# Kernel optimization log

Measured on AMD Instinct MI355X. Metric: run time of the kernel, lower is better.

The kernel has to match this reference:

```python
import jax, jax.numpy as jnp
import numpy as np

D, NH, DH, NL, NP, NLAYERS, DFF = 256, 8, 32, 3, 4, 6, 1024
SHAPES = ((64, 64), (32, 32), (16, 16))  # (H, W) per level, strides 8/16/32 of a 512px image


def layer_norm(x, g, b):
    m = jnp.mean(x, -1, keepdims=True)
    v = jnp.mean((x - m) ** 2, -1, keepdims=True)
    return (x - m) * jax.lax.rsqrt(v + 1e-5) * g + b


def _ref_points():
    pts = []
    for (h, w) in SHAPES:
        ry = (jnp.arange(h, dtype=jnp.float32) + 0.5) / h
        rx = (jnp.arange(w, dtype=jnp.float32) + 0.5) / w
        yy, xx = jnp.meshgrid(ry, rx, indexing='ij')
        pts.append(jnp.stack([xx.reshape(-1), yy.reshape(-1)], -1))
    return jnp.concatenate(pts, 0)  # [Q, 2] (x, y) normalized; valid_ratios == 1


def _sample_level(value_l, loc, h, w):
    # value_l: [B, NH, h*w, DH]; loc: [B, Q, NH, NP, 2] normalized in [0,1]
    # grid_sample(align_corners=False, padding zeros): pixel = loc*size - 0.5
    B, Q = loc.shape[0], loc.shape[1]
    x = loc[..., 0] * w - 0.5
    y = loc[..., 1] * h - 0.5
    x0f = jnp.floor(x); y0f = jnp.floor(y)
    lx = x - x0f; ly = y - y0f
    x0 = x0f.astype(jnp.int32); y0 = y0f.astype(jnp.int32)
    out = jnp.zeros((B, NH, Q, NP, DH), value_l.dtype)
    corners = ((0, 0, (1 - lx) * (1 - ly)), (1, 0, lx * (1 - ly)),
               (0, 1, (1 - lx) * ly), (1, 1, lx * ly))
    for dx, dy, wgt in corners:
        xi = x0 + dx; yi = y0 + dy
        valid = ((xi >= 0) & (xi < w) & (yi >= 0) & (yi < h)).astype(value_l.dtype)
        idx = jnp.clip(yi, 0, h - 1) * w + jnp.clip(xi, 0, w - 1)        # [B,Q,NH,NP]
        idx_f = jnp.transpose(idx, (0, 2, 1, 3)).reshape(B, NH, Q * NP)
        v = jnp.take_along_axis(value_l, idx_f[..., None], axis=2)       # [B,NH,Q*NP,DH]
        v = v.reshape(B, NH, Q, NP, DH)
        w_f = jnp.transpose(wgt * valid, (0, 2, 1, 3))                   # [B,NH,Q,NP]
        out = out + v * w_f[..., None]
    return out


def setup_inputs():
    key = jax.random.key(0)
    ks = iter(jax.random.split(key, 64))
    d = {}
    B = 4
    for i, (h, w) in enumerate(SHAPES):
        d[f'src{i}'] = jax.random.normal(next(ks), (B, D, h, w), jnp.float32)
        d[f'pos{i}'] = jax.random.normal(next(ks), (B, D, h, w), jnp.float32) * 0.1
    s = 0.02
    p = lambda shape: jax.random.normal(next(ks), shape, jnp.float32) * s
    d['level_embed'] = p((NL, D))
    d['W_off'] = p((NLAYERS, D, NH * NL * NP * 2)); d['b_off'] = p((NLAYERS, NH * NL * NP * 2))
    d['W_attn'] = p((NLAYERS, D, NH * NL * NP));   d['b_attn'] = p((NLAYERS, NH * NL * NP))
    d['W_val'] = p((NLAYERS, D, D)); d['b_val'] = p((NLAYERS, D))
    d['W_out'] = p((NLAYERS, D, D)); d['b_out'] = p((NLAYERS, D))
    d['ln1_g'] = jnp.ones((NLAYERS, D)); d['ln1_b'] = jnp.zeros((NLAYERS, D))
    d['W_ff1'] = p((NLAYERS, D, DFF)); d['b_ff1'] = p((NLAYERS, DFF))
    d['W_ff2'] = p((NLAYERS, DFF, D)); d['b_ff2'] = p((NLAYERS, D))
    d['ln2_g'] = jnp.ones((NLAYERS, D)); d['ln2_b'] = jnp.zeros((NLAYERS, D))
    return d


def reference(src0, src1, src2, pos0, pos1, pos2, level_embed,
              W_off, b_off, W_attn, b_attn, W_val, b_val, W_out, b_out,
              ln1_g, ln1_b, W_ff1, b_ff1, W_ff2, b_ff2, ln2_g, ln2_b):
    srcs = (src0, src1, src2)
    poss = (pos0, pos1, pos2)
    B = src0.shape[0]
    # flatten levels: [B, C, H, W] -> [B, H*W, C]; add per-level embedding to pos
    src = jnp.concatenate([s.reshape(B, D, -1).transpose(0, 2, 1) for s in srcs], 1)
    pos = jnp.concatenate([poss[l].reshape(B, D, -1).transpose(0, 2, 1) + level_embed[l]
                           for l in range(NL)], 1)
    Q = src.shape[1]
    ref = _ref_points()  # [Q, 2]
    x = src
    for i in range(NLAYERS):
        q = x + pos
        off = (q @ W_off[i] + b_off[i]).reshape(B, Q, NH, NL, NP, 2)
        aw = jax.nn.softmax((q @ W_attn[i] + b_attn[i]).reshape(B, Q, NH, NL * NP), -1)
        aw = aw.reshape(B, Q, NH, NL, NP)
        val = (x @ W_val[i] + b_val[i]).reshape(B, Q, NH, DH)
        attn_out = jnp.zeros((B, Q, NH, DH), x.dtype)
        start = 0
        for l, (h, w) in enumerate(SHAPES):
            hw = h * w
            v_l = jnp.transpose(val[:, start:start + hw], (0, 2, 1, 3))  # [B,NH,hw,DH]
            wh = jnp.array([w, h], jnp.float32)
            loc = ref[None, :, None, None, :] + off[:, :, :, l] / wh     # [B,Q,NH,NP,2]
            smp = _sample_level(v_l, loc, h, w)                          # [B,NH,Q,NP,DH]
            attn_out = attn_out + jnp.einsum('bhqpd,bqhp->bqhd', smp, aw[:, :, :, l])
            start += hw
        attn_out = attn_out.reshape(B, Q, D) @ W_out[i] + b_out[i]
        x = layer_norm(x + attn_out, ln1_g[i], ln1_b[i])
        ff = jax.nn.relu(x @ W_ff1[i] + b_ff1[i]) @ W_ff2[i] + b_ff2[i]
        x = layer_norm(x + ff, ln2_g[i], ln2_b[i])
    return x  # memory: [B, Q, D]
```

## Files before the change

kernel.cpp:

```cpp
#include <hip/hip_runtime.h>


#define DMODEL 256
#define NLAYERS 6
#define BATCH 4
#define QTOT 5376
#define MROWS (BATCH * QTOT)

typedef __bf16 bf16x8 __attribute__((ext_vector_type(8)));
typedef __bf16 bf16x4 __attribute__((ext_vector_type(4)));
typedef float floatx4 __attribute__((ext_vector_type(4)));

__global__ __launch_bounds__(256) void flatten_kernel(
    const float* __restrict__ s0, const float* __restrict__ p0,
    const float* __restrict__ s1, const float* __restrict__ p1,
    const float* __restrict__ s2, const float* __restrict__ p2,
    const float* __restrict__ lvl, float* __restrict__ x,
    float* __restrict__ pos, __bf16* __restrict__ xb,
    __bf16* __restrict__ qb) {
  __shared__ float ls[32][33];
  __shared__ float lp[32][33];
  int b = blockIdx.y;
  int tile = blockIdx.x;
  const float* sp; const float* pp; int l, hw, tp, td, qbase;
  if (tile < 1024)      { l = 0; hw = 4096; int t = tile;        td = t & 7; tp = t >> 3; qbase = 0; sp = s0; pp = p0; }
  else if (tile < 1280) { l = 1; hw = 1024; int t = tile - 1024; td = t & 7; tp = t >> 3; qbase = 4096; sp = s1; pp = p1; }
  else                  { l = 2; hw = 256;  int t = tile - 1280; td = t & 7; tp = t >> 3; qbase = 5120; sp = s2; pp = p2; }
  int tx = threadIdx.x & 31, ty = threadIdx.x >> 5;
  int d0 = td * 32, pbase = tp * 32;
#pragma unroll
  for (int r = 0; r < 4; ++r) {
    int dl = r * 8 + ty;
    size_t gi = ((size_t)(b * DMODEL + d0 + dl)) * hw + pbase + tx;
    ls[dl][tx] = sp[gi];
    lp[dl][tx] = pp[gi];
  }
  __syncthreads();
  int d = d0 + tx;
  float lv = lvl[l * DMODEL + d];
#pragma unroll
  for (int r = 0; r < 4; ++r) {
    int pl = r * 8 + ty;
    size_t bq = (size_t)b * QTOT + qbase + pbase + pl;
    float xv = ls[tx][pl];
    float pv = lp[tx][pl] + lv;
    x[bq * DMODEL + d] = xv;
    xb[bq * DMODEL + d] = (__bf16)xv;
    pos[bq * DMODEL + d] = pv;
    qb[bq * DMODEL + d] = (__bf16)(xv + pv);
  }
}

__global__ __launch_bounds__(256) void pack_wt_kernel(
    const float* __restrict__ W, __bf16* __restrict__ Wt, int K, int N) {
  int l = blockIdx.y;
  int idx = blockIdx.x * 256 + threadIdx.x;
  int n = idx / K, k = idx - n * K;
  Wt[(size_t)l * N * K + idx] = (__bf16)W[(size_t)l * K * N + (size_t)k * N + n];
}

__global__ __launch_bounds__(256) void pack_qv_kernel(
    const float* __restrict__ Woff, const float* __restrict__ Wattn,
    const float* __restrict__ Wval,
    const float* __restrict__ boff, const float* __restrict__ battn,
    const float* __restrict__ bval,
    __bf16* __restrict__ Wt, float* __restrict__ bc) {
  int l = blockIdx.y;
  int n = blockIdx.x;
  int k = threadIdx.x;
  float v = 0.f;
  if (n < 192)      v = Woff[((size_t)l * 256 + k) * 192 + n];
  else if (n < 288) v = Wattn[((size_t)l * 256 + k) * 96 + (n - 192)];
  else if (n >= 384) v = Wval[((size_t)l * 256 + k) * 256 + (n - 384)];
  Wt[((size_t)l * 640 + n) * 256 + k] = (__bf16)v;
  if (k == 0) {
    float b = 0.f;
    if (n < 192)      b = boff[l * 192 + n];
    else if (n < 288) b = battn[l * 96 + (n - 192)];
    else if (n >= 384) b = bval[l * 256 + (n - 384)];
    bc[l * 640 + n] = b;
  }
}

#define GEMM_CORE(A_, B_, K_)                                                  \
  for (int k0 = 0; k0 < (K_); k0 += 32) {                                      \
    __syncthreads();                                                           \
    _Pragma("unroll")                                                          \
    for (int cc = 0; cc < 2; ++cc) {                                           \
      int c = wid * 2 + cc;                                                    \
      __builtin_amdgcn_global_load_lds(                                        \
          (__attribute__((address_space(1))) void*)((A_) + (size_t)c * 16 * (K_) + k0), \
          (__attribute__((address_space(3))) void*)(As + c * 512), 16, 0, 0);  \
      __builtin_amdgcn_global_load_lds(                                        \
          (__attribute__((address_space(1))) void*)((B_) + (size_t)c * 16 * (K_) + k0), \
          (__attribute__((address_space(3))) void*)(Bs + c * 512), 16, 0, 0);  \
    }                                                                          \
    __syncthreads();                                                           \
    bf16x8 af[4], bfr[4];                                                      \
    _Pragma("unroll")                                                          \
    for (int i = 0; i < 4; ++i)                                                \
      af[i] = *(const bf16x8*)&As[(wr * 64 + i * 16 + (lane & 15)) * 32 + (lane >> 4) * 8]; \
    _Pragma("unroll")                                                          \
    for (int j = 0; j < 4; ++j)                                                \
      bfr[j] = *(const bf16x8*)&Bs[(wc * 64 + j * 16 + (lane & 15)) * 32 + (lane >> 4) * 8]; \
    _Pragma("unroll")                                                          \
    for (int i = 0; i < 4; ++i)                                                \
      _Pragma("unroll")                                                        \
      for (int j = 0; j < 4; ++j)                                              \
        acc[i][j] = __builtin_amdgcn_mfma_f32_16x16x32_bf16(af[i], bfr[j], acc[i][j], 0, 0, 0); \
  }

template<int RELU, int BF16OUT>
__global__ __launch_bounds__(256) void gemm_bf16_kernel(
    const __bf16* __restrict__ A, const __bf16* __restrict__ Wt,
    const float* __restrict__ bias, float* __restrict__ C,
    __bf16* __restrict__ Cb, int N, int K) {
  __shared__ __bf16 As[128 * 32];
  __shared__ __bf16 Bs[128 * 32];
  int t = threadIdx.x;
  int lane = t & 63, wid = t >> 6;
  int wr = wid >> 1, wc = wid & 1;
  int row0 = blockIdx.y * 128;
  int n0 = blockIdx.x * 128;
  floatx4 acc[4][4] = {};
  int srow = lane >> 2;
  int skoff = (lane & 3) * 8;
  const __bf16* Abase = A + (size_t)(row0 + srow) * K + skoff;
  const __bf16* Bbase = Wt + (size_t)(n0 + srow) * K + skoff;
  GEMM_CORE(Abase, Bbase, K)
  int orow = row0 + wr * 64 + (lane >> 4) * 4;
  int ocol = n0 + wc * 64 + (lane & 15);
#pragma unroll
  for (int i = 0; i < 4; ++i)
#pragma unroll
    for (int j = 0; j < 4; ++j) {
      int col = ocol + j * 16;
      float bv = bias[col];
#pragma unroll
      for (int r = 0; r < 4; ++r) {
        int row = orow + i * 16 + r;
        float v = acc[i][j][r] + bv;
        if (RELU) v = fmaxf(v, 0.f);
        if (BF16OUT) Cb[(size_t)row * N + col] = (__bf16)v;
        else         C[(size_t)row * N + col] = v;
      }
    }
}

__global__ __launch_bounds__(256) void gemm_qv_kernel(
    const __bf16* __restrict__ qb, const __bf16* __restrict__ xb,
    const __bf16* __restrict__ Wt, const float* __restrict__ bias,
    float* __restrict__ qproj, __bf16* __restrict__ valb) {
  __shared__ __bf16 As[128 * 32];
  __shared__ __bf16 Bs[128 * 32];
  int t = threadIdx.x;
  int lane = t & 63, wid = t >> 6;
  int wr = wid >> 1, wc = wid & 1;
  int bn = blockIdx.x;
  int row0 = blockIdx.y * 128;
  int n0 = bn * 128;
  const __bf16* A = (bn < 3) ? qb : xb;
  floatx4 acc[4][4] = {};
  int srow = lane >> 2;
  int skoff = (lane & 3) * 8;
  const __bf16* Abase = A + (size_t)(row0 + srow) * 256 + skoff;
  const __bf16* Bbase = Wt + (size_t)(n0 + srow) * 256 + skoff;
  GEMM_CORE(Abase, Bbase, 256)
  int orow = row0 + wr * 64 + (lane >> 4) * 4;
  int ocol = wc * 64 + (lane & 15);
#pragma unroll
  for (int i = 0; i < 4; ++i)
#pragma unroll
    for (int j = 0; j < 4; ++j) {
      int col = ocol + j * 16;
      float bv = bias[n0 + col];
#pragma unroll
      for (int r = 0; r < 4; ++r) {
        int row = orow + i * 16 + r;
        float v = acc[i][j][r] + bv;
        if (bn < 3) qproj[(size_t)row * 384 + n0 + col] = v;
        else        valb[(size_t)row * 256 + (n0 - 384) + col] = (__bf16)v;
      }
    }
}

__global__ __launch_bounds__(256) void deform_kernel(
    const __bf16* __restrict__ val, const float* __restrict__ qproj,
    __bf16* __restrict__ out) {
  int bq = blockIdx.x * 8 + (threadIdx.x >> 5);
  int b = bq / QTOT, q = bq % QTOT;
  int tq = threadIdx.x & 31;
  int hid = tq >> 2, dq = (tq & 3) * 8;

  int p, wsrc;
  if (q < 4096)      { p = q;        wsrc = 64; }
  else if (q < 5120) { p = q - 4096; wsrc = 32; }
  else               { p = q - 5120; wsrc = 16; }
  float inv = 1.0f / (float)wsrc;
  float refx = ((float)(p % wsrc) + 0.5f) * inv;
  float refy = ((float)(p / wsrc) + 0.5f) * inv;

  const float* base = qproj + (size_t)bq * 384;
  float aw[12], ob[24];
  *(float4*)&aw[0] = *(const float4*)(base + 192 + hid * 12);
  *(float4*)&aw[4] = *(const float4*)(base + 192 + hid * 12 + 4);
  *(float4*)&aw[8] = *(const float4*)(base + 192 + hid * 12 + 8);
#pragma unroll
  for (int i = 0; i < 6; ++i)
    *(float4*)&ob[i * 4] = *(const float4*)(base + hid * 24 + i * 4);

  float mx = -1e30f;
#pragma unroll
  for (int k = 0; k < 12; ++k) mx = fmaxf(mx, aw[k]);
  float s = 0.f;
#pragma unroll
  for (int k = 0; k < 12; ++k) { aw[k] = __expf(aw[k] - mx); s += aw[k]; }
  float invs = 1.0f / s;
#pragma unroll
  for (int k = 0; k < 12; ++k) aw[k] *= invs;

  const __bf16* vb = val + ((size_t)b * QTOT) * DMODEL + hid * 32 + dq;

  const int starts[3] = {0, 4096, 5120};
  const int wls[3] = {64, 32, 16};
  float acc[8] = {};
#pragma unroll
  for (int l = 0; l < 3; ++l) {
    int wl = wls[l], start = starts[l];
    float fwl = (float)wl;
#pragma unroll
    for (int pp = 0; pp < 4; ++pp) {
      float wcomb = aw[l * 4 + pp];
      float fx = refx * fwl + ob[(l * 4 + pp) * 2 + 0] - 0.5f;
      float fy = refy * fwl + ob[(l * 4 + pp) * 2 + 1] - 0.5f;
      float x0f = floorf(fx), y0f = floorf(fy);
      float lx = fx - x0f, ly = fy - y0f;
      int x0 = (int)x0f, y0 = (int)y0f;
#pragma unroll
      for (int c = 0; c < 4; ++c) {
        int dx = c & 1, dy = c >> 1;
        int xi = x0 + dx, yi = y0 + dy;
        if (xi >= 0 && xi < wl && yi >= 0 && yi < wl) {
          float wgt = (dx ? lx : 1.f - lx) * (dy ? ly : 1.f - ly) * wcomb;
          bf16x8 v = *(const bf16x8*)(vb + (size_t)(start + yi * wl + xi) * DMODEL);
#pragma unroll
          for (int e = 0; e < 8; ++e)
            acc[e] = fmaf(wgt, (float)v[e], acc[e]);
        }
      }
    }
  }
  bf16x8 o;
#pragma unroll
  for (int e = 0; e < 8; ++e) o[e] = (__bf16)acc[e];
  *(bf16x8*)(out + (size_t)bq * DMODEL + hid * 32 + dq) = o;
}

__global__ __launch_bounds__(256) void add_ln_kernel(
    const float* __restrict__ x, const float* __restrict__ res,
    const float* __restrict__ g, const float* __restrict__ bta,
    float* __restrict__ xout, __bf16* __restrict__ xb,
    const float* __restrict__ pos, __bf16* __restrict__ qb) {
  int row = blockIdx.x * 4 + (threadIdx.x >> 6);
  int lane = threadIdx.x & 63;
  float4 xv = ((const float4*)(x + (size_t)row * DMODEL))[lane];
  float4 rv = ((const float4*)(res + (size_t)row * DMODEL))[lane];
  xv.x += rv.x; xv.y += rv.y; xv.z += rv.z; xv.w += rv.w;
  float s = xv.x + xv.y + xv.z + xv.w;
  float sq = xv.x * xv.x + xv.y * xv.y + xv.z * xv.z + xv.w * xv.w;
#pragma unroll
  for (int o = 32; o >= 1; o >>= 1) {
    s += __shfl_xor(s, o);
    sq += __shfl_xor(sq, o);
  }
  float mean = s * (1.f / 256.f);
  float var = sq * (1.f / 256.f) - mean * mean;
  float rstd = rsqrtf(var + 1e-5f);
  int c = lane * 4;
  float4 gv = *(const float4*)(g + c);
  float4 bv = *(const float4*)(bta + c);
  float4 o4;
  o4.x = (xv.x - mean) * rstd * gv.x + bv.x;
  o4.y = (xv.y - mean) * rstd * gv.y + bv.y;
  o4.z = (xv.z - mean) * rstd * gv.z + bv.z;
  o4.w = (xv.w - mean) * rstd * gv.w + bv.w;
  ((float4*)(xout + (size_t)row * DMODEL))[lane] = o4;
  bf16x4 ob;
  ob[0] = (__bf16)o4.x; ob[1] = (__bf16)o4.y;
  ob[2] = (__bf16)o4.z; ob[3] = (__bf16)o4.w;
  *(bf16x4*)&xb[(size_t)row * DMODEL + c] = ob;
  if (pos) {
    float4 pv = ((const float4*)(pos + (size_t)row * DMODEL))[lane];
    bf16x4 qv;
    qv[0] = (__bf16)(o4.x + pv.x); qv[1] = (__bf16)(o4.y + pv.y);
    qv[2] = (__bf16)(o4.z + pv.z); qv[3] = (__bf16)(o4.w + pv.w);
    *(bf16x4*)&qb[(size_t)row * DMODEL + c] = qv;
  }
}

extern "C" void kernel_launch(void* const* d_in, const int* in_sizes, int n_in,
                              void* d_out, int out_size, void* d_ws, size_t ws_size,
                              hipStream_t stream) {
  const float* src0 = (const float*)d_in[0];
  const float* pos0 = (const float*)d_in[1];
  const float* src1 = (const float*)d_in[2];
  const float* pos1 = (const float*)d_in[3];
  const float* src2 = (const float*)d_in[4];
  const float* pos2 = (const float*)d_in[5];
  const float* lvl  = (const float*)d_in[6];
  const float* W_off  = (const float*)d_in[7];
  const float* b_off  = (const float*)d_in[8];
  const float* W_attn = (const float*)d_in[9];
  const float* b_attn = (const float*)d_in[10];
  const float* W_val  = (const float*)d_in[11];
  const float* b_val  = (const float*)d_in[12];
  const float* W_out  = (const float*)d_in[13];
  const float* b_out  = (const float*)d_in[14];
  const float* ln1g = (const float*)d_in[15];
  const float* ln1b = (const float*)d_in[16];
  const float* W_ff1 = (const float*)d_in[17];
  const float* b_ff1 = (const float*)d_in[18];
  const float* W_ff2 = (const float*)d_in[19];
  const float* b_ff2 = (const float*)d_in[20];
  const float* ln2g = (const float*)d_in[21];
  const float* ln2b = (const float*)d_in[22];

  const size_t M = (size_t)MROWS;
  char* w = (char*)d_ws;
  float*  x     = (float*)w;                 w += M * 256 * 4;
  float*  pos   = (float*)w;                 w += M * 256 * 4;
  __bf16* xb    = (__bf16*)w;                w += M * 256 * 2;
  __bf16* qb    = (__bf16*)w;                w += M * 256 * 2;
  float*  qproj = (float*)w;                 w += M * 384 * 4;
  __bf16* valb  = (__bf16*)w;                w += M * 256 * 2;
  __bf16* ffh   = (__bf16*)w;                w += M * 1024 * 2;
  __bf16* wqv_t = (__bf16*)w;                w += (size_t)NLAYERS * 640 * 256 * 2;
  __bf16* wout_t= (__bf16*)w;                w += (size_t)NLAYERS * 256 * 256 * 2;
  __bf16* wff1_t= (__bf16*)w;                w += (size_t)NLAYERS * 1024 * 256 * 2;
  __bf16* wff2_t= (__bf16*)w;                w += (size_t)NLAYERS * 256 * 1024 * 2;
  float*  bqv   = (float*)w;                 w += (size_t)NLAYERS * 640 * 4;
  __bf16* attn_bf = qb;
  float*  proj  = (float*)ffh;
  float*  ffres = qproj;

  pack_qv_kernel<<<dim3(640, NLAYERS), 256, 0, stream>>>(
      W_off, W_attn, W_val, b_off, b_attn, b_val, wqv_t, bqv);
  pack_wt_kernel<<<dim3(256, NLAYERS), 256, 0, stream>>>(W_out, wout_t, 256, 256);
  pack_wt_kernel<<<dim3(1024, NLAYERS), 256, 0, stream>>>(W_ff1, wff1_t, 256, 1024);
  pack_wt_kernel<<<dim3(1024, NLAYERS), 256, 0, stream>>>(W_ff2, wff2_t, 1024, 256);

  flatten_kernel<<<dim3(1344, BATCH), 256, 0, stream>>>(
      src0, pos0, src1, pos1, src2, pos2, lvl, x, pos, xb, qb);

  const int MT = MROWS / 128;
  for (int i = 0; i < NLAYERS; ++i) {
    gemm_qv_kernel<<<dim3(5, MT), 256, 0, stream>>>(
        qb, xb, wqv_t + (size_t)i * 640 * 256, bqv + i * 640, qproj, valb);
    deform_kernel<<<MROWS / 8, 256, 0, stream>>>(valb, qproj, attn_bf);
    gemm_bf16_kernel<0, 0><<<dim3(2, MT), 256, 0, stream>>>(
        attn_bf, wout_t + (size_t)i * 256 * 256, b_out + i * 256, proj, nullptr, 256, 256);
    add_ln_kernel<<<MROWS / 4, 256, 0, stream>>>(
        x, proj, ln1g + i * 256, ln1b + i * 256, x, xb, nullptr, nullptr);
    gemm_bf16_kernel<1, 1><<<dim3(8, MT), 256, 0, stream>>>(
        xb, wff1_t + (size_t)i * 1024 * 256, b_ff1 + i * 1024, nullptr, ffh, 1024, 256);
    gemm_bf16_kernel<0, 0><<<dim3(2, MT), 256, 0, stream>>>(
        ffh, wff2_t + (size_t)i * 256 * 1024, b_ff2 + i * 256, ffres, nullptr, 256, 1024);
    float* xdst = (i == NLAYERS - 1) ? (float*)d_out : x;
    add_ln_kernel<<<MROWS / 4, 256, 0, stream>>>(
        x, ffres, ln2g + i * 256, ln2b + i * 256, xdst, xb, pos, qb);
  }
}
```

Before: 1.017 ms.

## Tile weight transposes, branchless deform sampling, bf16 GEMM outputs for residual

Replaces the strided per-element weight pack kernels with 32x32 shared-memory tiled transposes and a separate bias pack. Rewrites the deformable sampling inner loop to clamp indices and zero out-of-range weights, issuing four unconditional loads per point instead of branching per corner. Switches the out-projection and FF2 GEMMs to write bf16, and the add+layernorm kernel to read a bf16 residual, halving that traffic. This costs some residual precision.

```diff
diff --git a/kernel.cpp b/kernel.cpp
--- a/kernel.cpp
+++ b/kernel.cpp
@@ -10,6 +10,11 @@
 typedef __bf16 bf16x8 __attribute__((ext_vector_type(8)));
 typedef __bf16 bf16x4 __attribute__((ext_vector_type(4)));
 typedef float floatx4 __attribute__((ext_vector_type(4)));
+
+#define GLOAD(gp, lp)                                                          \
+  __builtin_amdgcn_global_load_lds(                                            \
+      (__attribute__((address_space(1))) void*)(gp),                           \
+      (__attribute__((address_space(3))) void*)(lp), 16, 0, 0)
 
 __global__ __launch_bounds__(256) void flatten_kernel(
     const float* __restrict__ s0, const float* __restrict__ p0,
@@ -51,35 +56,54 @@
   }
 }
 
-__global__ __launch_bounds__(256) void pack_wt_kernel(
+__global__ __launch_bounds__(256) void pack_t_kernel(
     const float* __restrict__ W, __bf16* __restrict__ Wt, int K, int N) {
-  int l = blockIdx.y;
-  int idx = blockIdx.x * 256 + threadIdx.x;
-  int n = idx / K, k = idx - n * K;
-  Wt[(size_t)l * N * K + idx] = (__bf16)W[(size_t)l * K * N + (size_t)k * N + n];
-}
-
-__global__ __launch_bounds__(256) void pack_qv_kernel(
+  __shared__ float ls[32][33];
+  int l = blockIdx.z;
+  int n0 = blockIdx.x * 32, k0 = blockIdx.y * 32;
+  int tx = threadIdx.x & 31, ty = threadIdx.x >> 5;
+  const float* src = W + (size_t)l * K * N;
+#pragma unroll
+  for (int r = 0; r < 4; ++r)
+    ls[ty + r * 8][tx] = src[(size_t)(k0 + ty + r * 8) * N + n0 + tx];
+  __syncthreads();
+  __bf16* dst = Wt + (size_t)l * N * K;
+#pragma unroll
+  for (int r = 0; r < 4; ++r)
+    dst[(size_t)(n0 + ty + r * 8) * K + k0 + tx] = (__bf16)ls[tx][ty + r * 8];
+}
+
+__global__ __launch_bounds__(256) void pack_qv_t_kernel(
     const float* __restrict__ Woff, const float* __restrict__ Wattn,
-    const float* __restrict__ Wval,
+    const float* __restrict__ Wval, __bf16* __restrict__ Wt) {
+  __shared__ float ls[32][33];
+  int l = blockIdx.z;
+  int tc = blockIdx.x, k0 = blockIdx.y * 32;
+  int tx = threadIdx.x & 31, ty = threadIdx.x >> 5;
+  const float* src; int n0, sn;
+  if (tc < 6)       { src = Woff  + (size_t)l * 256 * 192; n0 = tc * 32;        sn = 192; }
+  else if (tc < 9)  { src = Wattn + (size_t)l * 256 * 96;  n0 = (tc - 6) * 32;  sn = 96;  }
+  else if (tc < 12) { src = nullptr; n0 = 0; sn = 0; }
+  else              { src = Wval  + (size_t)l * 256 * 256; n0 = (tc - 12) * 32; sn = 256; }
+#pragma unroll
+  for (int r = 0; r < 4; ++r)
+    ls[ty + r * 8][tx] = src ? src[(size_t)(k0 + ty + r * 8) * sn + n0 + tx] : 0.f;
+  __syncthreads();
+  __bf16* dst = Wt + (size_t)l * 640 * 256 + (size_t)tc * 32 * 256;
+#pragma unroll
+  for (int r = 0; r < 4; ++r)
+    dst[(size_t)(ty + r * 8) * 256 + k0 + tx] = (__bf16)ls[tx][ty + r * 8];
+}
+
+__global__ __launch_bounds__(640) void pack_bias_kernel(
     const float* __restrict__ boff, const float* __restrict__ battn,
-    const float* __restrict__ bval,
-    __bf16* __restrict__ Wt, float* __restrict__ bc) {
-  int l = blockIdx.y;
-  int n = blockIdx.x;
-  int k = threadIdx.x;
-  float v = 0.f;
-  if (n < 192)      v = Woff[((size_t)l * 256 + k) * 192 + n];
-  else if (n < 288) v = Wattn[((size_t)l * 256 + k) * 96 + (n - 192)];
-  else if (n >= 384) v = Wval[((size_t)l * 256 + k) * 256 + (n - 384)];
-  Wt[((size_t)l * 640 + n) * 256 + k] = (__bf16)v;
-  if (k == 0) {
-    float b = 0.f;
-    if (n < 192)      b = boff[l * 192 + n];
-    else if (n < 288) b = battn[l * 96 + (n - 192)];
-    else if (n >= 384) b = bval[l * 256 + (n - 384)];
-    bc[l * 640 + n] = b;
-  }
+    const float* __restrict__ bval, float* __restrict__ bc) {
+  int l = blockIdx.x, n = threadIdx.x;
+  float b = 0.f;
+  if (n < 192)       b = boff[l * 192 + n];
+  else if (n < 288)  b = battn[l * 96 + (n - 192)];
+  else if (n >= 384) b = bval[l * 256 + (n - 384)];
+  bc[l * 640 + n] = b;
 }
 
 #define GEMM_CORE(A_, B_, K_)                                                  \
@@ -88,12 +112,8 @@
     _Pragma("unroll")                                                          \
     for (int cc = 0; cc < 2; ++cc) {                                           \
       int c = wid * 2 + cc;                                                    \
-      __builtin_amdgcn_global_load_lds(                                        \
-          (__attribute__((address_space(1))) void*)((A_) + (size_t)c * 16 * (K_) + k0), \
-          (__attribute__((address_space(3))) void*)(As + c * 512), 16, 0, 0);  \
-      __builtin_amdgcn_global_load_lds(                                        \
-          (__attribute__((address_space(1))) void*)((B_) + (size_t)c * 16 * (K_) + k0), \
-          (__attribute__((address_space(3))) void*)(Bs + c * 512), 16, 0, 0);  \
+      GLOAD((A_) + (size_t)c * 16 * (K_) + k0, As + c * 512);                  \
+      GLOAD((B_) + (size_t)c * 16 * (K_) + k0, Bs + c * 512);                  \
     }                                                                          \
     __syncthreads();                                                           \
     bf16x8 af[4], bfr[4];                                                      \
@@ -226,27 +246,38 @@
   float acc[8] = {};
 #pragma unroll
   for (int l = 0; l < 3; ++l) {
-    int wl = wls[l], start = starts[l];
+    int wl = wls[l];
     float fwl = (float)wl;
+    const __bf16* vlb = vb + (size_t)starts[l] * DMODEL;
 #pragma unroll
     for (int pp = 0; pp < 4; ++pp) {
-      float wcomb = aw[l * 4 + pp];
+      float awp = aw[l * 4 + pp];
       float fx = refx * fwl + ob[(l * 4 + pp) * 2 + 0] - 0.5f;
       float fy = refy * fwl + ob[(l * 4 + pp) * 2 + 1] - 0.5f;
       float x0f = floorf(fx), y0f = floorf(fy);
       float lx = fx - x0f, ly = fy - y0f;
       int x0 = (int)x0f, y0 = (int)y0f;
-#pragma unroll
-      for (int c = 0; c < 4; ++c) {
-        int dx = c & 1, dy = c >> 1;
-        int xi = x0 + dx, yi = y0 + dy;
-        if (xi >= 0 && xi < wl && yi >= 0 && yi < wl) {
-          float wgt = (dx ? lx : 1.f - lx) * (dy ? ly : 1.f - ly) * wcomb;
-          bf16x8 v = *(const bf16x8*)(vb + (size_t)(start + yi * wl + xi) * DMODEL);
-#pragma unroll
-          for (int e = 0; e < 8; ++e)
-            acc[e] = fmaf(wgt, (float)v[e], acc[e]);
-        }
+      float wx0 = ((unsigned)x0 < (unsigned)wl) ? (1.f - lx) : 0.f;
+      float wx1 = ((unsigned)(x0 + 1) < (unsigned)wl) ? lx : 0.f;
+      float wy0 = (((unsigned)y0 < (unsigned)wl) ? (1.f - ly) : 0.f) * awp;
+      float wy1 = (((unsigned)(y0 + 1) < (unsigned)wl) ? ly : 0.f) * awp;
+      int xc0 = min(max(x0, 0), wl - 1);
+      int xc1 = min(max(x0 + 1, 0), wl - 1);
+      int yc0 = min(max(y0, 0), wl - 1);
+      int yc1 = min(max(y0 + 1, 0), wl - 1);
+      const __bf16* r0 = vlb + (size_t)(yc0 * wl) * DMODEL;
+      const __bf16* r1 = vlb + (size_t)(yc1 * wl) * DMODEL;
+      bf16x8 v00 = *(const bf16x8*)(r0 + (size_t)xc0 * DMODEL);
+      bf16x8 v01 = *(const bf16x8*)(r0 + (size_t)xc1 * DMODEL);
+      bf16x8 v10 = *(const bf16x8*)(r1 + (size_t)xc0 * DMODEL);
+      bf16x8 v11 = *(const bf16x8*)(r1 + (size_t)xc1 * DMODEL);
+      float w00 = wx0 * wy0, w01 = wx1 * wy0;
+      float w10 = wx0 * wy1, w11 = wx1 * wy1;
+#pragma unroll
+      for (int e = 0; e < 8; ++e) {
+        float v = w00 * (float)v00[e] + w01 * (float)v01[e] +
+                  w10 * (float)v10[e] + w11 * (float)v11[e];
+        acc[e] += v;
       }
     }
   }
@@ -257,15 +288,16 @@
 }
 
 __global__ __launch_bounds__(256) void add_ln_kernel(
-    const float* __restrict__ x, const float* __restrict__ res,
+    const float* __restrict__ x, const __bf16* __restrict__ res,
     const float* __restrict__ g, const float* __restrict__ bta,
     float* __restrict__ xout, __bf16* __restrict__ xb,
     const float* __restrict__ pos, __bf16* __restrict__ qb) {
   int row = blockIdx.x * 4 + (threadIdx.x >> 6);
   int lane = threadIdx.x & 63;
   float4 xv = ((const float4*)(x + (size_t)row * DMODEL))[lane];
-  float4 rv = ((const float4*)(res + (size_t)row * DMODEL))[lane];
-  xv.x += rv.x; xv.y += rv.y; xv.z += rv.z; xv.w += rv.w;
+  bf16x4 rv = ((const bf16x4*)(res + (size_t)row * DMODEL))[lane];
+  xv.x += (float)rv[0]; xv.y += (float)rv[1];
+  xv.z += (float)rv[2]; xv.w += (float)rv[3];
   float s = xv.x + xv.y + xv.z + xv.w;
   float sq = xv.x * xv.x + xv.y * xv.y + xv.z * xv.z + xv.w * xv.w;
 #pragma unroll
@@ -340,14 +372,14 @@
   __bf16* wff2_t= (__bf16*)w;                w += (size_t)NLAYERS * 256 * 1024 * 2;
   float*  bqv   = (float*)w;                 w += (size_t)NLAYERS * 640 * 4;
   __bf16* attn_bf = qb;
-  float*  proj  = (float*)ffh;
-  float*  ffres = qproj;
-
-  pack_qv_kernel<<<dim3(640, NLAYERS), 256, 0, stream>>>(
-      W_off, W_attn, W_val, b_off, b_attn, b_val, wqv_t, bqv);
-  pack_wt_kernel<<<dim3(256, NLAYERS), 256, 0, stream>>>(W_out, wout_t, 256, 256);
-  pack_wt_kernel<<<dim3(1024, NLAYERS), 256, 0, stream>>>(W_ff1, wff1_t, 256, 1024);
-  pack_wt_kernel<<<dim3(1024, NLAYERS), 256, 0, stream>>>(W_ff2, wff2_t, 1024, 256);
+  __bf16* proj  = ffh;
+  __bf16* ffres = (__bf16*)qproj;
+
+  pack_qv_t_kernel<<<dim3(20, 8, NLAYERS), 256, 0, stream>>>(W_off, W_attn, W_val, wqv_t);
+  pack_bias_kernel<<<NLAYERS, 640, 0, stream>>>(b_off, b_attn, b_val, bqv);
+  pack_t_kernel<<<dim3(8, 8, NLAYERS), 256, 0, stream>>>(W_out, wout_t, 256, 256);
+  pack_t_kernel<<<dim3(32, 8, NLAYERS), 256, 0, stream>>>(W_ff1, wff1_t, 256, 1024);
+  pack_t_kernel<<<dim3(8, 32, NLAYERS), 256, 0, stream>>>(W_ff2, wff2_t, 1024, 256);
 
   flatten_kernel<<<dim3(1344, BATCH), 256, 0, stream>>>(
       src0, pos0, src1, pos1, src2, pos2, lvl, x, pos, xb, qb);
@@ -357,14 +389,14 @@
     gemm_qv_kernel<<<dim3(5, MT), 256, 0, stream>>>(
         qb, xb, wqv_t + (size_t)i * 640 * 256, bqv + i * 640, qproj, valb);
     deform_kernel<<<MROWS / 8, 256, 0, stream>>>(valb, qproj, attn_bf);
-    gemm_bf16_kernel<0, 0><<<dim3(2, MT), 256, 0, stream>>>(
-        attn_bf, wout_t + (size_t)i * 256 * 256, b_out + i * 256, proj, nullptr, 256, 256);
+    gemm_bf16_kernel<0, 1><<<dim3(2, MT), 256, 0, stream>>>(
+        attn_bf, wout_t + (size_t)i * 256 * 256, b_out + i * 256, nullptr, proj, 256, 256);
     add_ln_kernel<<<MROWS / 4, 256, 0, stream>>>(
         x, proj, ln1g + i * 256, ln1b + i * 256, x, xb, nullptr, nullptr);
     gemm_bf16_kernel<1, 1><<<dim3(8, MT), 256, 0, stream>>>(
         xb, wff1_t + (size_t)i * 1024 * 256, b_ff1 + i * 1024, nullptr, ffh, 1024, 256);
-    gemm_bf16_kernel<0, 0><<<dim3(2, MT), 256, 0, stream>>>(
-        ffh, wff2_t + (size_t)i * 256 * 1024, b_ff2 + i * 256, ffres, nullptr, 256, 1024);
+    gemm_bf16_kernel<0, 1><<<dim3(2, MT), 256, 0, stream>>>(
+        ffh, wff2_t + (size_t)i * 256 * 1024, b_ff2 + i * 256, nullptr, ffres, 256, 1024);
     float* xdst = (i == NLAYERS - 1) ? (float*)d_out : x;
     add_ln_kernel<<<MROWS / 4, 256, 0, stream>>>(
         x, ffres, ln2g + i * 256, ln2b + i * 256, xdst, xb, pos, qb);
```

Result: faster. 925.5 us (-9.0%).
